# Performance work log

Hardware: AMD Instinct MI355X
Metric: run time of the kernel (lower is better)

Reference implementation:

```python
import jax, jax.numpy as jnp
import numpy as np

B, C, K, D = 2048, 100, 8, 64


def setup_inputs() -> dict:
    key = jax.random.key(0)
    k1, k2, k3, k4 = jax.random.split(key, 4)
    representation = jax.random.normal(k1, (B, D), dtype=jnp.float32)
    mixture_logits = 0.1 * jax.random.normal(k2, (C, K), dtype=jnp.float32)
    loc = jax.random.normal(k3, (C, K, D), dtype=jnp.float32)
    # lower-triangular with unit diagonal, small off-diagonal (matches 'random'/'zeros' init style)
    raw = 0.05 * jax.random.normal(k4, (C, K, D, D), dtype=jnp.float32)
    scale_tril = jnp.tril(raw, k=-1) + jnp.eye(D, dtype=jnp.float32)
    return {"representation": representation, "mixture_logits": mixture_logits,
            "loc": loc, "scale_tril": scale_tril}


def reference(representation, mixture_logits, loc, scale_tril):
    # representation: [B, D]; mixture_logits: [C, K]; loc: [C, K, D]; scale_tril: [C, K, D, D]
    d = representation.shape[-1]
    log2pi = jnp.log(jnp.asarray(2.0 * np.pi, dtype=representation.dtype))
    # residuals: [B, C, K, D] -> move batch last for batched triangular solve: [C, K, D, B]
    diff = representation[:, None, None, :] - loc[None]
    b = jnp.moveaxis(diff, 0, -1)
    # whiten: solve L z = (x - mu) for each (class, component)
    z = jax.lax.linalg.triangular_solve(scale_tril, b, left_side=True, lower=True)  # [C, K, D, B]
    quad = jnp.sum(z * z, axis=2)  # [C, K, B]
    # log|det Sigma|^{1/2} = sum log |diag(L)|
    logdet = jnp.sum(jnp.log(jnp.abs(jnp.diagonal(scale_tril, axis1=-2, axis2=-1))), axis=-1)  # [C, K]
    comp_lp = -0.5 * (quad + d * log2pi) - logdet[..., None]  # [C, K, B]
    mix = jax.nn.log_softmax(mixture_logits, axis=-1)  # [C, K]
    class_lp = jax.scipy.special.logsumexp(comp_lp + mix[..., None], axis=1)  # [C, B]
    logits = jax.nn.log_softmax(class_lp.T, axis=1)  # [B, C]
    return logits
```

## Files before the change

kernel.cpp:

```cpp
#include <hip/hip_runtime.h>
#include <math.h>

#define C_ 100
#define K_ 8
#define D_ 64
#define B_ 2048

using f16x8 = __attribute__((ext_vector_type(8))) _Float16;
using f32x4 = __attribute__((ext_vector_type(4))) float;

#define LS_S 68
#define AT_S 65
__global__ __launch_bounds__(64, 1) void k_invert(const float* __restrict__ L_g,
                                                  const float* __restrict__ loc_g,
                                                  const float* __restrict__ ml,
                                                  f16x8* __restrict__ ATf,
                                                  float* __restrict__ v_g,
                                                  float* __restrict__ off_g) {
    const int ck = blockIdx.x;
    const int j = threadIdx.x;
    __shared__ float Ls[D_][LS_S];
    __shared__ float At[D_][AT_S];
    __shared__ float mus[D_];

    {
        const int c8 = (ck >> 3) << 3;
        const float mlj = ml[c8 + (j & 7)];
        float mx = mlj;
        mx = fmaxf(mx, __shfl_xor(mx, 1, 64));
        mx = fmaxf(mx, __shfl_xor(mx, 2, 64));
        mx = fmaxf(mx, __shfl_xor(mx, 4, 64));
        float se = __expf(mlj - mx);
        se += __shfl_xor(se, 1, 64);
        se += __shfl_xor(se, 2, 64);
        se += __shfl_xor(se, 4, 64);
        const float lse = mx + __logf(se);
        if (j == (ck & 7)) off_g[ck] = mlj - lse - 58.8120661251f;
    }

    const float* Lsrc = L_g + (size_t)ck * D_ * D_;
#pragma unroll
    for (int t = 0; t < D_; ++t)
        Ls[t][j] = Lsrc[t * D_ + j];
    mus[j] = loc_g[ck * D_ + j];
    __syncthreads();

    float a[D_];
#pragma unroll
    for (int m = 0; m < D_; ++m) a[m] = (j == m) ? 1.f : 0.f;

#pragma unroll
    for (int i = 1; i < D_; ++i) {
        float a0 = 0.f, a1 = 0.f, a2 = 0.f, a3 = 0.f;
#pragma unroll
        for (int m0 = 0; m0 + 3 < i; m0 += 4) {
            const float4 L4 = *reinterpret_cast<const float4*>(&Ls[i][m0]);
            a0 = fmaf(L4.x, a[m0 + 0], a0);
            a1 = fmaf(L4.y, a[m0 + 1], a1);
            a2 = fmaf(L4.z, a[m0 + 2], a2);
            a3 = fmaf(L4.w, a[m0 + 3], a3);
        }
#pragma unroll
        for (int m = i & ~3; m < i; ++m) a0 = fmaf(Ls[i][m], a[m], a0);
        const float nv = -((a0 + a1) + (a2 + a3));
        a[i] = (j < i) ? nv : a[i];
    }

#pragma unroll
    for (int m = 0; m < D_; ++m) At[m][j] = a[m];
    __syncthreads();

    const int q8 = (j >> 4) * 8, cl = j & 15;
    float vpart[4];
#pragma unroll
    for (int dt = 0; dt < 4; ++dt) {
        vpart[dt] = 0.f;
#pragma unroll
        for (int ks = 0; ks < 2; ++ks) {
            f16x8 t;
#pragma unroll
            for (int s = 0; s < 8; ++s) {
                const _Float16 h = (_Float16)At[dt * 16 + cl][ks * 32 + q8 + s];
                t[s] = h;
                vpart[dt] = fmaf((float)h, mus[ks * 32 + q8 + s], vpart[dt]);
            }
            ATf[(size_t)ck * 512 + (dt * 2 + ks) * 64 + j] = t;
        }
        vpart[dt] += __shfl_xor(vpart[dt], 16, 64);
        vpart[dt] += __shfl_xor(vpart[dt], 32, 64);
    }
    if (j < 16) {
#pragma unroll
        for (int dt = 0; dt < 4; ++dt)
            v_g[(size_t)ck * D_ + dt * 16 + j] = vpart[dt];
    }
}

__global__ __launch_bounds__(256, 4) void k_main(const float* __restrict__ rep,
                                                 const f16x8* __restrict__ ATf,
                                                 const float* __restrict__ v_g,
                                                 const float* __restrict__ off_g,
                                                 float* __restrict__ clp_g) {
    const int c = blockIdx.y;
    const int b0 = blockIdx.x * 128;
    const int tid = threadIdx.x;
    const int w = tid >> 6;
    const int lane = tid & 63;
    const int col = lane & 15;
    const int quad = lane >> 4;

    __shared__ f16x8 Xs[1024];
    __shared__ float qk[K_][132];
    __shared__ float offs_s[K_];

    if (tid < K_) offs_s[tid] = off_g[c * K_ + tid];

#pragma unroll
    for (int p = 0; p < 4; ++p) {
        const int u = p * 256 + tid;
        const int q = u & 7, row = u >> 3;
        const float* xr = rep + (size_t)(b0 + row) * D_ + q * 8;
        const float4 x0 = *reinterpret_cast<const float4*>(xr);
        const float4 x1 = *reinterpret_cast<const float4*>(xr + 4);
        f16x8 val;
        val[0] = (_Float16)x0.x; val[1] = (_Float16)x0.y;
        val[2] = (_Float16)x0.z; val[3] = (_Float16)x0.w;
        val[4] = (_Float16)x1.x; val[5] = (_Float16)x1.y;
        val[6] = (_Float16)x1.z; val[7] = (_Float16)x1.w;
        const int s = row >> 5, bt = (row >> 4) & 1, cc = row & 15;
        Xs[((s * 2 + bt) * 8 + q) * 16 + (q ^ cc)] = val;
    }
    __syncthreads();

#pragma unroll 1
    for (int half = 0; half < 2; ++half) {
        const int k = w + half * 4;
        const int ck = c * K_ + k;
        f16x8 Af[8];
#pragma unroll
        for (int f = 0; f < 8; ++f)
            Af[f] = ATf[(size_t)ck * 512 + f * 64 + lane];
        f32x4 vvn[4];
#pragma unroll
        for (int dt = 0; dt < 4; ++dt)
            vvn[dt] = -(*reinterpret_cast<const f32x4*>(
                v_g + (size_t)ck * D_ + dt * 16 + quad * 4));

#pragma unroll 1
        for (int s = 0; s < 4; ++s) {
            f16x8 Xf[2][2];
#pragma unroll
            for (int bt = 0; bt < 2; ++bt)
#pragma unroll
                for (int ks = 0; ks < 2; ++ks) {
                    const int q = ks * 4 + quad;
                    Xf[bt][ks] = Xs[((s * 2 + bt) * 8 + q) * 16 + (q ^ col)];
                }

            f32x4 acc[2][4];
#pragma unroll
            for (int bt = 0; bt < 2; ++bt)
#pragma unroll
                for (int dt = 0; dt < 4; ++dt) {
                    acc[bt][dt] = __builtin_amdgcn_mfma_f32_16x16x32_f16(
                        Af[dt * 2 + 0], Xf[bt][0], vvn[dt], 0, 0, 0);
                    acc[bt][dt] = __builtin_amdgcn_mfma_f32_16x16x32_f16(
                        Af[dt * 2 + 1], Xf[bt][1], acc[bt][dt], 0, 0, 0);
                }

#pragma unroll
            for (int bt = 0; bt < 2; ++bt) {
                float p = 0.f;
#pragma unroll
                for (int dt = 0; dt < 4; ++dt)
#pragma unroll
                    for (int r = 0; r < 4; ++r)
                        p = fmaf(acc[bt][dt][r], acc[bt][dt][r], p);
                p += __shfl_xor(p, 16, 64);
                p += __shfl_xor(p, 32, 64);
                if (quad == 0)
                    qk[k][s * 32 + bt * 16 + col] = p;
            }
        }
    }
    __syncthreads();

    if (tid < 128) {
        float lp[K_];
        float m = -INFINITY;
#pragma unroll
        for (int k = 0; k < K_; ++k) {
            lp[k] = fmaf(-0.5f, qk[k][tid], offs_s[k]);
            m = fmaxf(m, lp[k]);
        }
        float s = 0.f;
#pragma unroll
        for (int k = 0; k < K_; ++k) s += __expf(lp[k] - m);
        clp_g[(size_t)c * B_ + b0 + tid] = m + __logf(s);
    }
}

__global__ __launch_bounds__(256) void k_final(const float* __restrict__ clp,
                                               float* __restrict__ out) {
    const int wave = threadIdx.x >> 6;
    const int lane = threadIdx.x & 63;
    const int b = blockIdx.x * 4 + wave;
    const float x0 = clp[(size_t)lane * B_ + b];
    const float x1 = (lane < C_ - 64) ? clp[(size_t)(64 + lane) * B_ + b] : -INFINITY;
    float m = fmaxf(x0, x1);
    for (int o = 32; o > 0; o >>= 1) m = fmaxf(m, __shfl_xor(m, o, 64));
    float s = __expf(x0 - m) + ((lane < C_ - 64) ? __expf(x1 - m) : 0.f);
    for (int o = 32; o > 0; o >>= 1) s += __shfl_xor(s, o, 64);
    const float L = m + __logf(s);
    out[(size_t)b * C_ + lane] = x0 - L;
    if (lane < C_ - 64) out[(size_t)b * C_ + 64 + lane] = x1 - L;
}

extern "C" void kernel_launch(void* const* d_in, const int* in_sizes, int n_in,
                              void* d_out, int out_size, void* d_ws, size_t ws_size,
                              hipStream_t stream) {
    const float* rep = (const float*)d_in[0];
    const float* ml  = (const float*)d_in[1];
    const float* loc = (const float*)d_in[2];
    const float* st  = (const float*)d_in[3];
    float* out = (float*)d_out;

    char* w = (char*)d_ws;
    f16x8* ATf = (f16x8*)w;
    float* v   = (float*)(w + 6553600);
    float* off = (float*)(w + 6758400);
    float* clp = (float*)(w + 6761600);

    k_invert<<<dim3(C_ * K_), dim3(64), 0, stream>>>(st, loc, ml, ATf, v, off);
    k_main<<<dim3(B_ / 128, C_), dim3(256), 0, stream>>>(rep, ATf, v, off, clp);
    k_final<<<dim3(B_ / 4), dim3(256), 0, stream>>>(clp, out);
}
```

Measured before the change: 100.6 us.

## Fuse final log-softmax into main kernel via last-block counter; two classes per block

The final class log-softmax kernel is folded into k_main. A per-batch-tile atomic counter elects the last finishing block, which then reduces all 100 class log-probs for its 128 rows and writes the output. Each k_main block now handles two classes, so X staging is shared across them and the grid is halved. k_invert reads L rows straight from global memory instead of staging them in shared memory. This removes a kernel launch and a sync but adds a memset, threadfences and a serial tail reduction done by only 16 blocks.

```diff
diff --git a/kernel.cpp b/kernel.cpp
--- a/kernel.cpp
+++ b/kernel.cpp
@@ -9,7 +9,6 @@
 using f16x8 = __attribute__((ext_vector_type(8))) _Float16;
 using f32x4 = __attribute__((ext_vector_type(4))) float;
 
-#define LS_S 68
 #define AT_S 65
 __global__ __launch_bounds__(64, 1) void k_invert(const float* __restrict__ L_g,
                                                   const float* __restrict__ loc_g,
@@ -19,7 +18,6 @@
                                                   float* __restrict__ off_g) {
     const int ck = blockIdx.x;
     const int j = threadIdx.x;
-    __shared__ float Ls[D_][LS_S];
     __shared__ float At[D_][AT_S];
     __shared__ float mus[D_];
 
@@ -38,12 +36,9 @@
         if (j == (ck & 7)) off_g[ck] = mlj - lse - 58.8120661251f;
     }
 
+    mus[j] = loc_g[ck * D_ + j];
+
     const float* Lsrc = L_g + (size_t)ck * D_ * D_;
-#pragma unroll
-    for (int t = 0; t < D_; ++t)
-        Ls[t][j] = Lsrc[t * D_ + j];
-    mus[j] = loc_g[ck * D_ + j];
-    __syncthreads();
 
     float a[D_];
 #pragma unroll
@@ -51,17 +46,18 @@
 
 #pragma unroll
     for (int i = 1; i < D_; ++i) {
+        const float* Lrow = Lsrc + i * D_;
         float a0 = 0.f, a1 = 0.f, a2 = 0.f, a3 = 0.f;
 #pragma unroll
         for (int m0 = 0; m0 + 3 < i; m0 += 4) {
-            const float4 L4 = *reinterpret_cast<const float4*>(&Ls[i][m0]);
+            const float4 L4 = *reinterpret_cast<const float4*>(Lrow + m0);
             a0 = fmaf(L4.x, a[m0 + 0], a0);
             a1 = fmaf(L4.y, a[m0 + 1], a1);
             a2 = fmaf(L4.z, a[m0 + 2], a2);
             a3 = fmaf(L4.w, a[m0 + 3], a3);
         }
 #pragma unroll
-        for (int m = i & ~3; m < i; ++m) a0 = fmaf(Ls[i][m], a[m], a0);
+        for (int m = i & ~3; m < i; ++m) a0 = fmaf(Lrow[m], a[m], a0);
         const float nv = -((a0 + a1) + (a2 + a3));
         a[i] = (j < i) ? nv : a[i];
     }
@@ -100,8 +96,10 @@
                                                  const f16x8* __restrict__ ATf,
                                                  const float* __restrict__ v_g,
                                                  const float* __restrict__ off_g,
-                                                 float* __restrict__ clp_g) {
-    const int c = blockIdx.y;
+                                                 float* __restrict__ clp_g,
+                                                 int* __restrict__ cnt,
+                                                 float* __restrict__ out) {
+    const int c0 = blockIdx.y * 2;
     const int b0 = blockIdx.x * 128;
     const int tid = threadIdx.x;
     const int w = tid >> 6;
@@ -110,10 +108,8 @@
     const int quad = lane >> 4;
 
     __shared__ f16x8 Xs[1024];
-    __shared__ float qk[K_][132];
-    __shared__ float offs_s[K_];
-
-    if (tid < K_) offs_s[tid] = off_g[c * K_ + tid];
+    __shared__ float qk[2][K_][132];
+    __shared__ int last_s;
 
 #pragma unroll
     for (int p = 0; p < 4; ++p) {
@@ -133,9 +129,10 @@
     __syncthreads();
 
 #pragma unroll 1
-    for (int half = 0; half < 2; ++half) {
+    for (int iter = 0; iter < 4; ++iter) {
+        const int cls = iter >> 1, half = iter & 1;
         const int k = w + half * 4;
-        const int ck = c * K_ + k;
+        const int ck = (c0 + cls) * K_ + k;
         f16x8 Af[8];
 #pragma unroll
         for (int f = 0; f < 8; ++f)
@@ -179,41 +176,55 @@
                 p += __shfl_xor(p, 16, 64);
                 p += __shfl_xor(p, 32, 64);
                 if (quad == 0)
-                    qk[k][s * 32 + bt * 16 + col] = p;
+                    qk[cls][k][s * 32 + bt * 16 + col] = p;
             }
         }
     }
     __syncthreads();
 
-    if (tid < 128) {
+    {
+        const int cls = tid >> 7, row = tid & 127;
+        const float* offp = off_g + (c0 + cls) * K_;
         float lp[K_];
         float m = -INFINITY;
 #pragma unroll
         for (int k = 0; k < K_; ++k) {
-            lp[k] = fmaf(-0.5f, qk[k][tid], offs_s[k]);
+            lp[k] = fmaf(-0.5f, qk[cls][k][row], offp[k]);
             m = fmaxf(m, lp[k]);
         }
         float s = 0.f;
 #pragma unroll
         for (int k = 0; k < K_; ++k) s += __expf(lp[k] - m);
-        clp_g[(size_t)c * B_ + b0 + tid] = m + __logf(s);
-    }
-}
-
-__global__ __launch_bounds__(256) void k_final(const float* __restrict__ clp,
-                                               float* __restrict__ out) {
-    const int wave = threadIdx.x >> 6;
-    const int lane = threadIdx.x & 63;
-    const int b = blockIdx.x * 4 + wave;
-    const float x0 = clp[(size_t)lane * B_ + b];
-    const float x1 = (lane < C_ - 64) ? clp[(size_t)(64 + lane) * B_ + b] : -INFINITY;
-    float m = fmaxf(x0, x1);
-    for (int o = 32; o > 0; o >>= 1) m = fmaxf(m, __shfl_xor(m, o, 64));
-    float s = __expf(x0 - m) + ((lane < C_ - 64) ? __expf(x1 - m) : 0.f);
-    for (int o = 32; o > 0; o >>= 1) s += __shfl_xor(s, o, 64);
-    const float L = m + __logf(s);
-    out[(size_t)b * C_ + lane] = x0 - L;
-    if (lane < C_ - 64) out[(size_t)b * C_ + 64 + lane] = x1 - L;
+        clp_g[(size_t)(c0 + cls) * B_ + b0 + row] = m + __logf(s);
+    }
+
+    __threadfence();
+    __syncthreads();
+    if (tid == 0)
+        last_s = (atomicAdd(&cnt[blockIdx.x], 1) == (int)gridDim.y - 1) ? 1 : 0;
+    __syncthreads();
+    if (last_s) {
+        __threadfence();
+        float* red = (float*)qk;
+        const int row = tid & 127;
+        const int ch = tid >> 7;
+        const float* base = clp_g + b0 + row;
+        float m = -INFINITY;
+        for (int c = ch * 50; c < ch * 50 + 50; ++c)
+            m = fmaxf(m, base[(size_t)c * B_]);
+        red[ch * 128 + row] = m;
+        __syncthreads();
+        const float mm = fmaxf(red[row], red[128 + row]);
+        float s = 0.f;
+        for (int c = ch * 50; c < ch * 50 + 50; ++c)
+            s += __expf(base[(size_t)c * B_] - mm);
+        red[256 + ch * 128 + row] = s;
+        __syncthreads();
+        const float L = mm + __logf(red[256 + row] + red[256 + 128 + row]);
+        float* orow = out + (size_t)(b0 + row) * C_ + ch * 50;
+        for (int c = 0; c < 50; ++c)
+            orow[c] = base[(size_t)(ch * 50 + c) * B_] - L;
+    }
 }
 
 extern "C" void kernel_launch(void* const* d_in, const int* in_sizes, int n_in,
@@ -230,8 +241,10 @@
     float* v   = (float*)(w + 6553600);
     float* off = (float*)(w + 6758400);
     float* clp = (float*)(w + 6761600);
-
+    int*   cnt = (int*)(w + 7580800);
+
+    hipMemsetAsync(cnt, 0, (B_ / 128) * sizeof(int), stream);
     k_invert<<<dim3(C_ * K_), dim3(64), 0, stream>>>(st, loc, ml, ATf, v, off);
-    k_main<<<dim3(B_ / 128, C_), dim3(256), 0, stream>>>(rep, ATf, v, off, clp);
-    k_final<<<dim3(B_ / 4), dim3(256), 0, stream>>>(clp, out);
+    k_main<<<dim3(B_ / 128, C_ / 2), dim3(256), 0, stream>>>(rep, ATf, v, off,
+                                                             clp, cnt, out);
 }
```

New measurement: 199.2 us. +98.1%, slower.
